# Kernel optimization log

Measured on AMD Instinct MI355X. Metric: run time of the kernel, lower is better.

The kernel has to match this reference:

```python
import jax, jax.numpy as jnp
import numpy as np

SIZE = 128
B, S = 32, 8192


def setup_inputs() -> dict:
    key = jax.random.key(0)
    kx, = jax.random.split(key, 1)
    x = jax.random.normal(kx, (B, S, SIZE), dtype=jnp.float32)
    return {
        "x": x,
        # DyT params
        "alpha": jnp.ones((1,), jnp.float32) * 0.5,
        "dyt_weight": jnp.ones((SIZE,), jnp.float32),
        "dyt_bias": jnp.zeros((SIZE,), jnp.float32),
        # FourierForwardNetwork params
        "a_real": jnp.ones((SIZE,), jnp.float32),
        "a_imag": jnp.zeros((SIZE,), jnp.float32),
        "b_real": jnp.ones((SIZE,), jnp.float32),
        "b_imag": jnp.zeros((SIZE,), jnp.float32),
        "ffn_bias": jnp.zeros((SIZE,), jnp.float32),
    }


def reference(x, alpha, dyt_weight, dyt_bias, a_real, a_imag, b_real, b_imag, ffn_bias):
    # DyT: tanh(alpha * x) * weight + bias
    h = jnp.tanh(alpha * x) * dyt_weight + dyt_bias  # [B, S, SIZE]
    # FourierForwardNetwork. NOTE: in the original torch code the first
    # spectral branch (multiply by a, ifft, +bias, gelu) is DEAD CODE --
    # its result is overwritten by `X = torch.fft.fft(x + 0j)`. The actual
    # output is ifft(fft(h) * b).real, reproduced faithfully here.
    b = b_real + 1j * b_imag  # [SIZE] complex
    X = jnp.fft.fft(h.astype(jnp.complex64), axis=-1)  # [B, S, SIZE] complex64
    y = jnp.fft.ifft(X * b, axis=-1).real.astype(x.dtype)
    # Residual connection of FourierFFNBlock
    return y + x
```

## Files before the change

### kernel.cpp

```cpp
#include <hip/hip_runtime.h>

#define SIZE 128
#define PAD 136

typedef short short8 __attribute__((ext_vector_type(8)));
typedef float f32x4 __attribute__((ext_vector_type(4)));

__device__ __forceinline__ unsigned short f2bf(float f) {
    unsigned int u = __float_as_uint(f);
    unsigned int r = u + 0x7FFFu + ((u >> 16) & 1u);
    return (unsigned short)(r >> 16);
}
__device__ __forceinline__ float bf2f(unsigned short h) {
    return __uint_as_float(((unsigned int)h) << 16);
}

__global__ void build_gt(const float* __restrict__ br, const float* __restrict__ bi,
                         const float* __restrict__ w, const float* __restrict__ bias,
                         unsigned short* __restrict__ Gt, float* __restrict__ C0) {
    __shared__ float gr[SIZE];
    const int t = threadIdx.x;
    float acc = 0.0f;
    for (int j = 0; j < SIZE; ++j) {
        int p = (j * t) & 127;
        float a = (float)p * (1.0f / 64.0f);
        acc += br[j] * cospif(a) - bi[j] * sinpif(a);
    }
    gr[t] = acc * (1.0f / 128.0f);
    __syncthreads();
    float c0 = 0.0f;
    for (int k = 0; k < SIZE; ++k) {
        const float g = gr[(t - k) & 127];
        c0 += bias[k] * g;
        Gt[t * SIZE + k] = f2bf(w[k] * g);
    }
    C0[t] = c0;
}

__global__ __launch_bounds__(256, 4) void fourier_main(
    const float* __restrict__ x, const float* __restrict__ alpha_p,
    const unsigned short* __restrict__ Gt, const float* __restrict__ C0,
    float* __restrict__ out) {
    __shared__ unsigned short hA[64 * PAD];
    __shared__ unsigned short oA[64 * PAD];

    const int tid = threadIdx.x;
    const int lane = tid & 63;
    const int wid = tid >> 6;
    const int lrow = lane & 15;
    const int slot = lane >> 4;
    const int colb = wid * 32;

    const float a2 = 2.0f * alpha_p[0];
    const unsigned base = (unsigned)blockIdx.x * (64u * SIZE);

    const int rl = tid >> 5;
    const int cl = (tid & 31) * 4;

    float4 xr[8];
#pragma unroll
    for (int j = 0; j < 8; ++j)
        xr[j] = *reinterpret_cast<const float4*>(&x[base + j * 1024 + tid * 4]);

#pragma unroll
    for (int j = 0; j < 8; ++j) {
        ushort4 hq;
        float e, r;
        e = __expf(a2 * xr[j].x); r = __builtin_amdgcn_rcpf(1.0f + e);
        hq.x = f2bf(fmaf(-2.0f, r, 1.0f));
        e = __expf(a2 * xr[j].y); r = __builtin_amdgcn_rcpf(1.0f + e);
        hq.y = f2bf(fmaf(-2.0f, r, 1.0f));
        e = __expf(a2 * xr[j].z); r = __builtin_amdgcn_rcpf(1.0f + e);
        hq.z = f2bf(fmaf(-2.0f, r, 1.0f));
        e = __expf(a2 * xr[j].w); r = __builtin_amdgcn_rcpf(1.0f + e);
        hq.w = f2bf(fmaf(-2.0f, r, 1.0f));
        *reinterpret_cast<ushort4*>(&hA[(j * 8 + rl) * PAD + cl]) = hq;
    }

    short8 gf[2][4];
    float4 c0v[2];
#pragma unroll
    for (int nt = 0; nt < 2; ++nt) {
        const int c = colb + nt * 16 + lrow;
#pragma unroll
        for (int kt = 0; kt < 4; ++kt)
            gf[nt][kt] = *reinterpret_cast<const short8*>(
                &Gt[c * SIZE + kt * 32 + slot * 8]);
        c0v[nt] = *reinterpret_cast<const float4*>(&C0[colb + nt * 16 + slot * 4]);
    }

    __syncthreads();

#pragma unroll
    for (int mt = 0; mt < 4; ++mt) {
        short8 hf[4];
#pragma unroll
        for (int kt = 0; kt < 4; ++kt)
            hf[kt] = *reinterpret_cast<const short8*>(
                &hA[(mt * 16 + lrow) * PAD + kt * 32 + slot * 8]);
#pragma unroll
        for (int nt = 0; nt < 2; ++nt) {
            f32x4 a = {0.f, 0.f, 0.f, 0.f};
#pragma unroll
            for (int kt = 0; kt < 4; ++kt)
                a = __builtin_amdgcn_mfma_f32_16x16x32_bf16(gf[nt][kt], hf[kt], a,
                                                            0, 0, 0);
            ushort4 o;
            o.x = f2bf(a[0] + c0v[nt].x);
            o.y = f2bf(a[1] + c0v[nt].y);
            o.z = f2bf(a[2] + c0v[nt].z);
            o.w = f2bf(a[3] + c0v[nt].w);
            *reinterpret_cast<ushort4*>(
                &oA[(mt * 16 + lrow) * PAD + colb + nt * 16 + slot * 4]) = o;
        }
    }

    __syncthreads();

#pragma unroll
    for (int j = 0; j < 8; ++j) {
        const ushort4 ov =
            *reinterpret_cast<const ushort4*>(&oA[(j * 8 + rl) * PAD + cl]);
        float4 r;
        r.x = bf2f(ov.x) + xr[j].x;
        r.y = bf2f(ov.y) + xr[j].y;
        r.z = bf2f(ov.z) + xr[j].z;
        r.w = bf2f(ov.w) + xr[j].w;
        *reinterpret_cast<float4*>(&out[base + j * 1024 + tid * 4]) = r;
    }
}

extern "C" void kernel_launch(void* const* d_in, const int* in_sizes, int n_in,
                              void* d_out, int out_size, void* d_ws, size_t ws_size,
                              hipStream_t stream) {
    const float* x = (const float*)d_in[0];
    const float* alpha = (const float*)d_in[1];
    const float* dyt_w = (const float*)d_in[2];
    const float* dyt_b = (const float*)d_in[3];
    const float* b_real = (const float*)d_in[6];
    const float* b_imag = (const float*)d_in[7];
    float* out = (float*)d_out;

    unsigned short* Gt = (unsigned short*)d_ws;
    float* C0 = (float*)((char*)d_ws + SIZE * SIZE * 2);

    build_gt<<<1, 128, 0, stream>>>(b_real, b_imag, dyt_w, dyt_b, Gt, C0);

    const int rows = out_size / SIZE;
    const int nblocks = rows / 64;
    fourier_main<<<nblocks, 256, 0, stream>>>(x, alpha, Gt, C0, out);
}
```

Before: 71.01 us.

## Give each wave its own 16 rows and drop block barriers

Restructures fourier_main so each wavefront processes 16 independent rows across all 128 output columns, instead of the four waves sharing 64 rows and splitting the columns. This removes both __syncthreads, halves LDS by reusing a single per-wave buffer for input and output, and raises the launch bound to 5 blocks per CU. The trade-off is that each wave now streams the full Gt matrix (8 column tiles) from cache rather than keeping a quarter of it in registers, which adds L1/L2 load traffic.

```diff
diff --git a/kernel.cpp b/kernel.cpp
--- a/kernel.cpp
+++ b/kernel.cpp
@@ -1,7 +1,7 @@
 #include <hip/hip_runtime.h>
 
 #define SIZE 128
-#define PAD 136
+#define PADW 136
 
 typedef short short8 __attribute__((ext_vector_type(8)));
 typedef float f32x4 __attribute__((ext_vector_type(4)));
@@ -37,30 +37,29 @@
     C0[t] = c0;
 }
 
-__global__ __launch_bounds__(256, 4) void fourier_main(
+__global__ __launch_bounds__(256, 5) void fourier_main(
     const float* __restrict__ x, const float* __restrict__ alpha_p,
     const unsigned short* __restrict__ Gt, const float* __restrict__ C0,
     float* __restrict__ out) {
-    __shared__ unsigned short hA[64 * PAD];
-    __shared__ unsigned short oA[64 * PAD];
+    __shared__ unsigned short hS[4][16][PADW];
 
     const int tid = threadIdx.x;
     const int lane = tid & 63;
-    const int wid = tid >> 6;
+    const int wv = tid >> 6;
     const int lrow = lane & 15;
     const int slot = lane >> 4;
-    const int colb = wid * 32;
 
     const float a2 = 2.0f * alpha_p[0];
-    const unsigned base = (unsigned)blockIdx.x * (64u * SIZE);
 
-    const int rl = tid >> 5;
-    const int cl = (tid & 31) * 4;
+    const unsigned base =
+        (unsigned)blockIdx.x * (64u * SIZE) + (unsigned)wv * (16u * SIZE);
+    const int rl = lane >> 5;
+    const int cl = (lane & 31) * 4;
 
     float4 xr[8];
 #pragma unroll
     for (int j = 0; j < 8; ++j)
-        xr[j] = *reinterpret_cast<const float4*>(&x[base + j * 1024 + tid * 4]);
+        xr[j] = *reinterpret_cast<const float4*>(&x[base + j * 256 + lane * 4]);
 
 #pragma unroll
     for (int j = 0; j < 8; ++j) {
@@ -74,59 +73,45 @@
         hq.z = f2bf(fmaf(-2.0f, r, 1.0f));
         e = __expf(a2 * xr[j].w); r = __builtin_amdgcn_rcpf(1.0f + e);
         hq.w = f2bf(fmaf(-2.0f, r, 1.0f));
-        *reinterpret_cast<ushort4*>(&hA[(j * 8 + rl) * PAD + cl]) = hq;
+        *reinterpret_cast<ushort4*>(&hS[wv][2 * j + rl][cl]) = hq;
     }
 
-    short8 gf[2][4];
-    float4 c0v[2];
+    short8 hf[4];
 #pragma unroll
-    for (int nt = 0; nt < 2; ++nt) {
-        const int c = colb + nt * 16 + lrow;
+    for (int kt = 0; kt < 4; ++kt)
+        hf[kt] = *reinterpret_cast<const short8*>(
+            &hS[wv][lrow][kt * 32 + slot * 8]);
+
+#pragma unroll
+    for (int nt = 0; nt < 8; ++nt) {
+        short8 gf[4];
 #pragma unroll
         for (int kt = 0; kt < 4; ++kt)
-            gf[nt][kt] = *reinterpret_cast<const short8*>(
-                &Gt[c * SIZE + kt * 32 + slot * 8]);
-        c0v[nt] = *reinterpret_cast<const float4*>(&C0[colb + nt * 16 + slot * 4]);
-    }
-
-    __syncthreads();
-
-#pragma unroll
-    for (int mt = 0; mt < 4; ++mt) {
-        short8 hf[4];
+            gf[kt] = *reinterpret_cast<const short8*>(
+                &Gt[(nt * 16 + lrow) * SIZE + kt * 32 + slot * 8]);
+        const float4 c0v = *reinterpret_cast<const float4*>(&C0[nt * 16 + slot * 4]);
+        f32x4 a = {0.f, 0.f, 0.f, 0.f};
 #pragma unroll
         for (int kt = 0; kt < 4; ++kt)
-            hf[kt] = *reinterpret_cast<const short8*>(
-                &hA[(mt * 16 + lrow) * PAD + kt * 32 + slot * 8]);
-#pragma unroll
-        for (int nt = 0; nt < 2; ++nt) {
-            f32x4 a = {0.f, 0.f, 0.f, 0.f};
-#pragma unroll
-            for (int kt = 0; kt < 4; ++kt)
-                a = __builtin_amdgcn_mfma_f32_16x16x32_bf16(gf[nt][kt], hf[kt], a,
-                                                            0, 0, 0);
-            ushort4 o;
-            o.x = f2bf(a[0] + c0v[nt].x);
-            o.y = f2bf(a[1] + c0v[nt].y);
-            o.z = f2bf(a[2] + c0v[nt].z);
-            o.w = f2bf(a[3] + c0v[nt].w);
-            *reinterpret_cast<ushort4*>(
-                &oA[(mt * 16 + lrow) * PAD + colb + nt * 16 + slot * 4]) = o;
-        }
+            a = __builtin_amdgcn_mfma_f32_16x16x32_bf16(gf[kt], hf[kt], a, 0, 0, 0);
+        ushort4 o;
+        o.x = f2bf(a[0] + c0v.x);
+        o.y = f2bf(a[1] + c0v.y);
+        o.z = f2bf(a[2] + c0v.z);
+        o.w = f2bf(a[3] + c0v.w);
+        *reinterpret_cast<ushort4*>(&hS[wv][lrow][nt * 16 + slot * 4]) = o;
     }
-
-    __syncthreads();
 
 #pragma unroll
     for (int j = 0; j < 8; ++j) {
         const ushort4 ov =
-            *reinterpret_cast<const ushort4*>(&oA[(j * 8 + rl) * PAD + cl]);
+            *reinterpret_cast<const ushort4*>(&hS[wv][2 * j + rl][cl]);
         float4 r;
         r.x = bf2f(ov.x) + xr[j].x;
         r.y = bf2f(ov.y) + xr[j].y;
         r.z = bf2f(ov.z) + xr[j].z;
         r.w = bf2f(ov.w) + xr[j].w;
-        *reinterpret_cast<float4*>(&out[base + j * 1024 + tid * 4]) = r;
+        *reinterpret_cast<float4*>(&out[base + j * 256 + lane * 4]) = r;
     }
 }
 
```

Result: slower. 145.4 us (+104.7%).

## Halve output LDS buffer by processing MFMA and epilogue in two halves

Applied to the files above, without the earlier changes.

Shrinks the bf16 output staging buffer from 64 to 32 rows by running the MFMA convolution and the residual-add epilogue in two halves separated by extra barriers. It also raises the launch-bounds occupancy hint from 4 to 6 blocks per CU. The aim is to cut LDS and register use so more blocks stay resident, which helps hide the memory latency of this bandwidth-bound kernel. In exchange it adds two block-wide barriers, and the tighter register budget could cause spills, since the eight float4 x values stay live throughout.

```diff
diff --git a/kernel.cpp b/kernel.cpp
--- a/kernel.cpp
+++ b/kernel.cpp
@@ -1,7 +1,7 @@
 #include <hip/hip_runtime.h>
 
 #define SIZE 128
-#define PAD 136
+#define PADW 136
 
 typedef short short8 __attribute__((ext_vector_type(8)));
 typedef float f32x4 __attribute__((ext_vector_type(4)));
@@ -37,12 +37,12 @@
     C0[t] = c0;
 }
 
-__global__ __launch_bounds__(256, 4) void fourier_main(
+__global__ __launch_bounds__(256, 6) void fourier_main(
     const float* __restrict__ x, const float* __restrict__ alpha_p,
     const unsigned short* __restrict__ Gt, const float* __restrict__ C0,
     float* __restrict__ out) {
-    __shared__ unsigned short hA[64 * PAD];
-    __shared__ unsigned short oA[64 * PAD];
+    __shared__ unsigned short hA[64 * PADW];
+    __shared__ unsigned short oA[32 * PADW];
 
     const int tid = threadIdx.x;
     const int lane = tid & 63;
@@ -74,7 +74,7 @@
         hq.z = f2bf(fmaf(-2.0f, r, 1.0f));
         e = __expf(a2 * xr[j].w); r = __builtin_amdgcn_rcpf(1.0f + e);
         hq.w = f2bf(fmaf(-2.0f, r, 1.0f));
-        *reinterpret_cast<ushort4*>(&hA[(j * 8 + rl) * PAD + cl]) = hq;
+        *reinterpret_cast<ushort4*>(&hA[(j * 8 + rl) * PADW + cl]) = hq;
     }
 
     short8 gf[2][4];
@@ -91,43 +91,53 @@
 
     __syncthreads();
 
+    auto conv_half = [&](int mt0) __attribute__((always_inline)) {
 #pragma unroll
-    for (int mt = 0; mt < 4; ++mt) {
-        short8 hf[4];
-#pragma unroll
-        for (int kt = 0; kt < 4; ++kt)
-            hf[kt] = *reinterpret_cast<const short8*>(
-                &hA[(mt * 16 + lrow) * PAD + kt * 32 + slot * 8]);
-#pragma unroll
-        for (int nt = 0; nt < 2; ++nt) {
-            f32x4 a = {0.f, 0.f, 0.f, 0.f};
+        for (int mt = mt0; mt < mt0 + 2; ++mt) {
+            short8 hf[4];
 #pragma unroll
             for (int kt = 0; kt < 4; ++kt)
-                a = __builtin_amdgcn_mfma_f32_16x16x32_bf16(gf[nt][kt], hf[kt], a,
-                                                            0, 0, 0);
-            ushort4 o;
-            o.x = f2bf(a[0] + c0v[nt].x);
-            o.y = f2bf(a[1] + c0v[nt].y);
-            o.z = f2bf(a[2] + c0v[nt].z);
-            o.w = f2bf(a[3] + c0v[nt].w);
-            *reinterpret_cast<ushort4*>(
-                &oA[(mt * 16 + lrow) * PAD + colb + nt * 16 + slot * 4]) = o;
+                hf[kt] = *reinterpret_cast<const short8*>(
+                    &hA[(mt * 16 + lrow) * PADW + kt * 32 + slot * 8]);
+#pragma unroll
+            for (int nt = 0; nt < 2; ++nt) {
+                f32x4 a = {0.f, 0.f, 0.f, 0.f};
+#pragma unroll
+                for (int kt = 0; kt < 4; ++kt)
+                    a = __builtin_amdgcn_mfma_f32_16x16x32_bf16(gf[nt][kt], hf[kt],
+                                                                a, 0, 0, 0);
+                ushort4 o;
+                o.x = f2bf(a[0] + c0v[nt].x);
+                o.y = f2bf(a[1] + c0v[nt].y);
+                o.z = f2bf(a[2] + c0v[nt].z);
+                o.w = f2bf(a[3] + c0v[nt].w);
+                *reinterpret_cast<ushort4*>(
+                    &oA[((mt - mt0) * 16 + lrow) * PADW + colb + nt * 16 +
+                        slot * 4]) = o;
+            }
         }
-    }
+    };
+    auto epi_half = [&](int j0) __attribute__((always_inline)) {
+#pragma unroll
+        for (int j = j0; j < j0 + 4; ++j) {
+            const ushort4 ov = *reinterpret_cast<const ushort4*>(
+                &oA[((j - j0) * 8 + rl) * PADW + cl]);
+            float4 r;
+            r.x = bf2f(ov.x) + xr[j].x;
+            r.y = bf2f(ov.y) + xr[j].y;
+            r.z = bf2f(ov.z) + xr[j].z;
+            r.w = bf2f(ov.w) + xr[j].w;
+            *reinterpret_cast<float4*>(&out[base + j * 1024 + tid * 4]) = r;
+        }
+    };
 
+    conv_half(0);
     __syncthreads();
-
-#pragma unroll
-    for (int j = 0; j < 8; ++j) {
-        const ushort4 ov =
-            *reinterpret_cast<const ushort4*>(&oA[(j * 8 + rl) * PAD + cl]);
-        float4 r;
-        r.x = bf2f(ov.x) + xr[j].x;
-        r.y = bf2f(ov.y) + xr[j].y;
-        r.z = bf2f(ov.z) + xr[j].z;
-        r.w = bf2f(ov.w) + xr[j].w;
-        *reinterpret_cast<float4*>(&out[base + j * 1024 + tid * 4]) = r;
-    }
+    epi_half(0);
+    __syncthreads();
+    conv_half(2);
+    __syncthreads();
+    epi_half(4);
 }
 
 extern "C" void kernel_launch(void* const* d_in, const int* in_sizes, int n_in,
```

Measured after the change: 136.3 us. +91.9%, slower.

## Stream x tiles into swizzled LDS with double-buffered async loads

Applied to the files above, without the earlier changes.

Each block now handles four 64-row tiles and prefetches the next tile from global memory straight into a double-buffered, XOR-swizzled LDS buffer using global_load_lds, overlapping loads with the tanh+MFMA work. The tanh is computed while reading MFMA fragments from LDS, and the residual add plus output store happen straight from the accumulators. This removes the bf16 output staging buffer and its extra LDS round trip and barrier. In exchange, fewer blocks are launched, occupancy is lower (launch bounds 2), and the output stores become 16-byte scattered writes per row instead of fully coalesced row-major writes.

```diff
diff --git a/kernel.cpp b/kernel.cpp
--- a/kernel.cpp
+++ b/kernel.cpp
@@ -1,7 +1,7 @@
 #include <hip/hip_runtime.h>
 
 #define SIZE 128
-#define PAD 136
+#define TPB 4
 
 typedef short short8 __attribute__((ext_vector_type(8)));
 typedef float f32x4 __attribute__((ext_vector_type(4)));
@@ -10,9 +10,6 @@
     unsigned int u = __float_as_uint(f);
     unsigned int r = u + 0x7FFFu + ((u >> 16) & 1u);
     return (unsigned short)(r >> 16);
-}
-__device__ __forceinline__ float bf2f(unsigned short h) {
-    return __uint_as_float(((unsigned int)h) << 16);
 }
 
 __global__ void build_gt(const float* __restrict__ br, const float* __restrict__ bi,
@@ -37,45 +34,27 @@
     C0[t] = c0;
 }
 
-__global__ __launch_bounds__(256, 4) void fourier_main(
+__device__ __forceinline__ void cp16_g2l(const float* g, float* l) {
+    __builtin_amdgcn_global_load_lds(
+        (const __attribute__((address_space(1))) unsigned int*)g,
+        (__attribute__((address_space(3))) unsigned int*)l, 16, 0, 0);
+}
+
+__global__ __launch_bounds__(256, 2) void fourier_main(
     const float* __restrict__ x, const float* __restrict__ alpha_p,
     const unsigned short* __restrict__ Gt, const float* __restrict__ C0,
     float* __restrict__ out) {
-    __shared__ unsigned short hA[64 * PAD];
-    __shared__ unsigned short oA[64 * PAD];
+    __shared__ float xs[2][64 * SIZE];
 
     const int tid = threadIdx.x;
     const int lane = tid & 63;
-    const int wid = tid >> 6;
+    const int wv = tid >> 6;
     const int lrow = lane & 15;
     const int slot = lane >> 4;
-    const int colb = wid * 32;
+    const int colb = wv * 32;
 
     const float a2 = 2.0f * alpha_p[0];
-    const unsigned base = (unsigned)blockIdx.x * (64u * SIZE);
-
-    const int rl = tid >> 5;
-    const int cl = (tid & 31) * 4;
-
-    float4 xr[8];
-#pragma unroll
-    for (int j = 0; j < 8; ++j)
-        xr[j] = *reinterpret_cast<const float4*>(&x[base + j * 1024 + tid * 4]);
-
-#pragma unroll
-    for (int j = 0; j < 8; ++j) {
-        ushort4 hq;
-        float e, r;
-        e = __expf(a2 * xr[j].x); r = __builtin_amdgcn_rcpf(1.0f + e);
-        hq.x = f2bf(fmaf(-2.0f, r, 1.0f));
-        e = __expf(a2 * xr[j].y); r = __builtin_amdgcn_rcpf(1.0f + e);
-        hq.y = f2bf(fmaf(-2.0f, r, 1.0f));
-        e = __expf(a2 * xr[j].z); r = __builtin_amdgcn_rcpf(1.0f + e);
-        hq.z = f2bf(fmaf(-2.0f, r, 1.0f));
-        e = __expf(a2 * xr[j].w); r = __builtin_amdgcn_rcpf(1.0f + e);
-        hq.w = f2bf(fmaf(-2.0f, r, 1.0f));
-        *reinterpret_cast<ushort4*>(&hA[(j * 8 + rl) * PAD + cl]) = hq;
-    }
+    const unsigned blockBase = (unsigned)blockIdx.x * (TPB * 64u * SIZE);
 
     short8 gf[2][4];
     float4 c0v[2];
@@ -89,44 +68,90 @@
         c0v[nt] = *reinterpret_cast<const float4*>(&C0[colb + nt * 16 + slot * 4]);
     }
 
-    __syncthreads();
+    const int rh = lane >> 5;
+    const int cc = lane & 31;
+    auto stage = [&](int t, int buf) __attribute__((always_inline)) {
+        const float* src = x + blockBase + (unsigned)t * (64u * SIZE);
+#pragma unroll
+        for (int i = 0; i < 8; ++i) {
+            const int r = 16 * wv + 2 * i + rh;
+            const float* g = src + (unsigned)r * SIZE + (unsigned)((cc ^ (r & 7)) << 2);
+            float* l = &xs[buf][(16 * wv + 2 * i) * SIZE];
+            cp16_g2l(g, l);
+        }
+    };
+
+    stage(0, 0);
 
 #pragma unroll
-    for (int mt = 0; mt < 4; ++mt) {
-        short8 hf[4];
+    for (int t = 0; t < TPB; ++t) {
+        __builtin_amdgcn_s_barrier();
+        if (t + 1 < TPB) stage(t + 1, (t + 1) & 1);
+
+        if (t + 1 < TPB) {
+            asm volatile("s_waitcnt vmcnt(8)" ::: "memory");
+        } else {
+            asm volatile("s_waitcnt vmcnt(0)" ::: "memory");
+        }
+        __builtin_amdgcn_sched_barrier(0);
+        __builtin_amdgcn_s_barrier();
+        __builtin_amdgcn_sched_barrier(0);
+
+        const float* xb = &xs[t & 1][0];
+        const unsigned tbase = blockBase + (unsigned)t * (64u * SIZE);
 #pragma unroll
-        for (int kt = 0; kt < 4; ++kt)
-            hf[kt] = *reinterpret_cast<const short8*>(
-                &hA[(mt * 16 + lrow) * PAD + kt * 32 + slot * 8]);
-#pragma unroll
-        for (int nt = 0; nt < 2; ++nt) {
-            f32x4 a = {0.f, 0.f, 0.f, 0.f};
+        for (int mt = 0; mt < 4; ++mt) {
+            const int r = mt * 16 + lrow;
+            const unsigned rb = (unsigned)r * SIZE;
+            const int sw = r & 7;
+
+            f32x4 xk[8];
 #pragma unroll
             for (int kt = 0; kt < 4; ++kt)
-                a = __builtin_amdgcn_mfma_f32_16x16x32_bf16(gf[nt][kt], hf[kt], a,
-                                                            0, 0, 0);
-            ushort4 o;
-            o.x = f2bf(a[0] + c0v[nt].x);
-            o.y = f2bf(a[1] + c0v[nt].y);
-            o.z = f2bf(a[2] + c0v[nt].z);
-            o.w = f2bf(a[3] + c0v[nt].w);
-            *reinterpret_cast<ushort4*>(
-                &oA[(mt * 16 + lrow) * PAD + colb + nt * 16 + slot * 4]) = o;
-        }
-    }
+#pragma unroll
+                for (int j = 0; j < 2; ++j) {
+                    const int chunk = kt * 8 + slot * 2 + j;
+                    xk[kt * 2 + j] = *reinterpret_cast<const f32x4*>(
+                        &xb[rb + (unsigned)((chunk ^ sw) << 2)]);
+                }
 
-    __syncthreads();
+            short8 hf[4];
+#pragma unroll
+            for (int kt = 0; kt < 4; ++kt) {
+                short8 h;
+#pragma unroll
+                for (int j = 0; j < 2; ++j) {
+                    const f32x4 v = xk[kt * 2 + j];
+#pragma unroll
+                    for (int e = 0; e < 4; ++e) {
+                        const float ex = __expf(a2 * v[e]);
+                        const float th =
+                            fmaf(-2.0f, __builtin_amdgcn_rcpf(1.0f + ex), 1.0f);
+                        h[j * 4 + e] = (short)f2bf(th);
+                    }
+                }
+                hf[kt] = h;
+            }
 
 #pragma unroll
-    for (int j = 0; j < 8; ++j) {
-        const ushort4 ov =
-            *reinterpret_cast<const ushort4*>(&oA[(j * 8 + rl) * PAD + cl]);
-        float4 r;
-        r.x = bf2f(ov.x) + xr[j].x;
-        r.y = bf2f(ov.y) + xr[j].y;
-        r.z = bf2f(ov.z) + xr[j].z;
-        r.w = bf2f(ov.w) + xr[j].w;
-        *reinterpret_cast<float4*>(&out[base + j * 1024 + tid * 4]) = r;
+            for (int nt = 0; nt < 2; ++nt) {
+                f32x4 a = {0.f, 0.f, 0.f, 0.f};
+#pragma unroll
+                for (int kt = 0; kt < 4; ++kt)
+                    a = __builtin_amdgcn_mfma_f32_16x16x32_bf16(gf[nt][kt], hf[kt],
+                                                                a, 0, 0, 0);
+                const int chunk_r = (colb >> 2) + nt * 4 + slot;
+                const f32x4 xa = *reinterpret_cast<const f32x4*>(
+                    &xb[rb + (unsigned)((chunk_r ^ sw) << 2)]);
+                float4 o;
+                o.x = a[0] + c0v[nt].x + xa[0];
+                o.y = a[1] + c0v[nt].y + xa[1];
+                o.z = a[2] + c0v[nt].z + xa[2];
+                o.w = a[3] + c0v[nt].w + xa[3];
+                *reinterpret_cast<float4*>(
+                    &out[tbase + rb + (unsigned)(chunk_r << 2)]) = o;
+            }
+        }
     }
 }
 
@@ -147,6 +172,6 @@
     build_gt<<<1, 128, 0, stream>>>(b_real, b_imag, dyt_w, dyt_b, Gt, C0);
 
     const int rows = out_size / SIZE;
-    const int nblocks = rows / 64;
+    const int nblocks = rows / (64 * TPB);
     fourier_main<<<nblocks, 256, 0, stream>>>(x, alpha, Gt, C0, out);
 }
```

After: 86.17 us. +21.3%, slower.
